# Kernel tuning notes

Measured on AMD Instinct MI355X. Metric: run time of the kernel, lower is better.

Reference implementation:

```python
import jax, jax.numpy as jnp
import numpy as np

NUM_SUBSET = 3
BN_EPS = 1e-5


def setup_inputs() -> dict:
    key = jax.random.key(0)
    ks = jax.random.split(key, 6)
    N, C, T, V = 32, 192, 256, 25
    x = jax.random.normal(ks[0], (N, C, T, V), dtype=jnp.float32)
    w_in = jax.random.normal(ks[1], (3 * C, C), dtype=jnp.float32) * (1.0 / np.sqrt(C))
    b_in = jax.random.normal(ks[2], (3 * C,), dtype=jnp.float32) * 0.02
    w_ff = jax.random.normal(ks[3], (C, C), dtype=jnp.float32) * (1.0 / np.sqrt(C))
    b_ff = jax.random.normal(ks[4], (C,), dtype=jnp.float32) * 0.02
    bn_gamma = jnp.ones((C,), dtype=jnp.float32)
    bn_beta = jnp.zeros((C,), dtype=jnp.float32)
    bn_mean = jnp.zeros((C,), dtype=jnp.float32)
    bn_var = jnp.ones((C,), dtype=jnp.float32)
    return dict(x=x, w_in=w_in, b_in=b_in, w_ff=w_ff, b_ff=b_ff,
                bn_gamma=bn_gamma, bn_beta=bn_beta, bn_mean=bn_mean, bn_var=bn_var)


def reference(x, w_in, b_in, w_ff, b_ff, bn_gamma, bn_beta, bn_mean, bn_var):
    N, C, T, V = x.shape
    S = NUM_SUBSET
    mid = C // S
    # 1x1 conv QKV projection: (N,C,T,V) x (3C,C) -> (N,3C,T,V)
    qkv = jnp.einsum('nctv,dc->ndtv', x, w_in) + b_in[None, :, None, None]
    qkv = qkv.reshape(N, 3 * S, mid, T, V)
    q, k, v = jnp.split(qkv, 3, axis=1)  # each (N,S,mid,T,V)
    # tanh-normalized attention over time: (N,S,T,T)
    att = jnp.tanh(jnp.einsum('nsctv,nscqv->nstq', q, k) / (mid * V))
    y = jnp.einsum('nstq,nscqv->nsctv', att, v).reshape(N, C, T, V)
    # ff_nett: 1x1 conv + BatchNorm (inference form)
    y = jnp.einsum('nctv,dc->ndtv', y, w_ff) + b_ff[None, :, None, None]
    inv = bn_gamma / jnp.sqrt(bn_var + BN_EPS)
    y = (y - bn_mean[None, :, None, None]) * inv[None, :, None, None] + bn_beta[None, :, None, None]
    # residual + LeakyReLU(0.1)
    z = x + y
    return jnp.where(z >= 0, z, 0.1 * z)
```

## Files before the change

kernel.cpp:

```cpp
#include <hip/hip_runtime.h>

#define TV 6400
#define NCH 192
#define D3 576

typedef unsigned short u16;
typedef unsigned int   u32;

typedef __attribute__((ext_vector_type(8))) short bf16x8;
typedef __attribute__((ext_vector_type(4))) float f32x4;

__device__ __forceinline__ float bf2f(u32 h) { return __uint_as_float(h << 16); }
__device__ __forceinline__ u16 f2bf(float f) {
    u32 u = __float_as_uint(f);
    return (u16)((u + 0x7FFFu + ((u >> 16) & 1u)) >> 16);
}

__global__ __launch_bounds__(256) void k_wcast(const float* __restrict__ w_in,
                                               const float* __restrict__ w_ff,
                                               u32* __restrict__ wb) {
    int i = blockIdx.x * 256 + threadIdx.x;
    float2 f;
    if (i < 55296) f = *(const float2*)(w_in + 2 * i);
    else           f = *(const float2*)(w_ff + 2 * (i - 55296));
    wb[i] = (u32)f2bf(f.x) | ((u32)f2bf(f.y) << 16);
}

__global__ __launch_bounds__(256) void k_qkv(const float* __restrict__ x,
                                             const u16* __restrict__ w_inb,
                                             const float* __restrict__ b_in,
                                             u16* __restrict__ qkv,
                                             u16* __restrict__ qt,
                                             u16* __restrict__ kt) {
    const int p0 = blockIdx.x * 64, n = blockIdx.y;
    const int tid = threadIdx.x;
    const int wid = tid >> 6, lane = tid & 63;
    const int wd = wid & 1, wp = wid >> 1;
    const int ml = lane & 15, kq = lane >> 4;

    __shared__ __align__(16) char Bs[64 * 384];
    __shared__ __align__(16) char As[64 * 384];
    float* L = (float*)As;

    for (int cc = 0; cc < 3; ++cc) {
        const float* xn = x + ((size_t)n * NCH + cc * 64) * TV + p0;
#pragma unroll
        for (int r = 0; r < 4; ++r) {
            int idx = tid + 256 * r;
            int c = idx >> 4, p4 = idx & 15;
            float4 v = *(const float4*)(xn + (size_t)c * TV + p4 * 4);
            *(float4*)&L[c * 65 + p4 * 4] = v;
        }
        __syncthreads();
        {
            int p = tid >> 2, cq = tid & 3;
            u32 buf[8];
#pragma unroll
            for (int j = 0; j < 8; ++j) {
                float f0 = L[(cq * 16 + 2 * j) * 65 + p];
                float f1 = L[(cq * 16 + 2 * j + 1) * 65 + p];
                buf[j] = (u32)f2bf(f0) | ((u32)f2bf(f1) << 16);
            }
#pragma unroll
            for (int h = 0; h < 2; ++h) {
                int g = cc * 8 + cq * 2 + h;
                uint4 u;
                u.x = buf[h * 4]; u.y = buf[h * 4 + 1];
                u.z = buf[h * 4 + 2]; u.w = buf[h * 4 + 3];
                *(uint4*)(Bs + p * 384 + (((g & ~7) | ((g ^ p) & 7)) << 4)) = u;
            }
        }
        __syncthreads();
    }

    for (int dt = 0; dt < 9; ++dt) {
#pragma unroll
        for (int r = 0; r < 6; ++r) {
            int idx = tid + 256 * r;
            int row = idx / 24, g = idx - row * 24;
            uint4 v = *(const uint4*)(w_inb + (size_t)(dt * 64 + row) * 192 + g * 8);
            *(uint4*)(As + row * 384 + (((g & ~7) | ((g ^ row) & 7)) << 4)) = v;
        }
        __syncthreads();

        f32x4 acc[2][2];
#pragma unroll
        for (int i = 0; i < 2; i++)
#pragma unroll
            for (int j = 0; j < 2; j++)
#pragma unroll
                for (int r = 0; r < 4; r++) acc[i][j][r] = 0.f;

#pragma unroll
        for (int kk = 0; kk < 3; ++kk)
#pragma unroll
            for (int ks = 0; ks < 2; ++ks) {
                int g = kk * 8 + ks * 4 + kq;
                bf16x8 aw[2], bx[2];
#pragma unroll
                for (int mt = 0; mt < 2; ++mt) {
                    int row = wd * 32 + mt * 16 + ml;
                    aw[mt] = *(const bf16x8*)(As + row * 384 + (((g & ~7) | ((g ^ row) & 7)) << 4));
                }
#pragma unroll
                for (int nt = 0; nt < 2; ++nt) {
                    int row = wp * 32 + nt * 16 + ml;
                    bx[nt] = *(const bf16x8*)(Bs + row * 384 + (((g & ~7) | ((g ^ row) & 7)) << 4));
                }
#pragma unroll
                for (int mt = 0; mt < 2; ++mt)
#pragma unroll
                    for (int nt = 0; nt < 2; ++nt)
                        acc[mt][nt] = __builtin_amdgcn_mfma_f32_16x16x32_bf16(aw[mt], bx[nt], acc[mt][nt], 0, 0, 0);
            }

        if (dt < 6) {
            const int s = (dt < 3) ? dt : dt - 3;
            u16* dstb = (dt < 3 ? qt : kt) + ((size_t)(n * 3 + s) * 6400 + p0) * 64;
#pragma unroll
            for (int mt = 0; mt < 2; ++mt) {
                int c = wd * 32 + mt * 16 + kq * 4;
                float4 bias = *(const float4*)(b_in + dt * 64 + c);
#pragma unroll
                for (int nt = 0; nt < 2; ++nt) {
                    int p = wp * 32 + nt * 16 + ml;
                    u32 w0 = (u32)f2bf(acc[mt][nt][0] + bias.x) | ((u32)f2bf(acc[mt][nt][1] + bias.y) << 16);
                    u32 w1 = (u32)f2bf(acc[mt][nt][2] + bias.z) | ((u32)f2bf(acc[mt][nt][3] + bias.w) << 16);
                    uint2 u; u.x = w0; u.y = w1;
                    *(uint2*)(dstb + (size_t)p * 64 + c) = u;
                }
            }
        } else {
#pragma unroll
            for (int mt = 0; mt < 2; ++mt) {
                int d = dt * 64 + wd * 32 + mt * 16 + kq * 4;
                float4 bias = *(const float4*)(b_in + d);
                u16* vdst = qkv + ((size_t)n * D3 + d) * TV;
#pragma unroll
                for (int nt = 0; nt < 2; ++nt) {
                    int p = p0 + wp * 32 + nt * 16 + ml;
                    vdst[(size_t)0 * TV + p] = f2bf(acc[mt][nt][0] + bias.x);
                    vdst[(size_t)1 * TV + p] = f2bf(acc[mt][nt][1] + bias.y);
                    vdst[(size_t)2 * TV + p] = f2bf(acc[mt][nt][2] + bias.z);
                    vdst[(size_t)3 * TV + p] = f2bf(acc[mt][nt][3] + bias.w);
                }
            }
        }
        __syncthreads();
    }
}

__global__ __launch_bounds__(256) void k_scores(const u16* __restrict__ qt,
                                                const u16* __restrict__ kt,
                                                u16* __restrict__ att) {
    const int b = blockIdx.z, t0 = blockIdx.y * 128, q0 = blockIdx.x * 64;
    const int tid = threadIdx.x;
    const int wid = tid >> 6, lane = tid & 63;
    const int wm = wid & 1, wn = wid >> 1;
    const int ml = lane & 15, kq = lane >> 4;

    __shared__ __align__(16) char As[128 * 128];
    __shared__ __align__(16) char Bs[64 * 128];

    f32x4 acc[4][2];
#pragma unroll
    for (int i = 0; i < 4; i++)
#pragma unroll
        for (int j = 0; j < 2; j++)
#pragma unroll
            for (int r = 0; r < 4; r++) acc[i][j][r] = 0.f;

    const u16* qb = qt + (size_t)b * 256 * 1600;
    const u16* kb = kt + (size_t)b * 256 * 1600;

    for (int kc = 0; kc < 1600; kc += 64) {
#pragma unroll
        for (int r = 0; r < 4; r++) {
            int idx = tid + 256 * r;
            int row = idx >> 3, g = idx & 7;
            uint4 v = *(const uint4*)(qb + (size_t)(t0 + row) * 1600 + kc + g * 8);
            *(uint4*)(As + row * 128 + (((g ^ row) & 7) << 4)) = v;
        }
#pragma unroll
        for (int r = 0; r < 2; r++) {
            int idx = tid + 256 * r;
            int row = idx >> 3, g = idx & 7;
            uint4 v = *(const uint4*)(kb + (size_t)(q0 + row) * 1600 + kc + g * 8);
            *(uint4*)(Bs + row * 128 + (((g ^ row) & 7) << 4)) = v;
        }
        __syncthreads();
#pragma unroll
        for (int ks = 0; ks < 2; ks++) {
            int gb = ks * 4 + kq;
            bf16x8 a[4], bb[2];
#pragma unroll
            for (int mt = 0; mt < 4; mt++) {
                int row = wm * 64 + mt * 16 + ml;
                a[mt] = *(const bf16x8*)(As + row * 128 + (((gb ^ row) & 7) << 4));
            }
#pragma unroll
            for (int nt = 0; nt < 2; nt++) {
                int row = wn * 32 + nt * 16 + ml;
                bb[nt] = *(const bf16x8*)(Bs + row * 128 + (((gb ^ row) & 7) << 4));
            }
#pragma unroll
            for (int mt = 0; mt < 4; mt++)
#pragma unroll
                for (int nt = 0; nt < 2; nt++)
                    acc[mt][nt] = __builtin_amdgcn_mfma_f32_16x16x32_bf16(a[mt], bb[nt], acc[mt][nt], 0, 0, 0);
        }
        __syncthreads();
    }

    const float sc = 1.0f / 1600.0f;
    u16* ab = att + (size_t)b * 65536;
#pragma unroll
    for (int mt = 0; mt < 4; mt++)
#pragma unroll
        for (int nt = 0; nt < 2; nt++) {
            int q = q0 + wn * 32 + nt * 16 + ml;
#pragma unroll
            for (int r = 0; r < 4; r++) {
                int t = t0 + wm * 64 + mt * 16 + kq * 4 + r;
                ab[(size_t)t * 256 + q] = f2bf(tanhf(acc[mt][nt][r] * sc));
            }
        }
}

__global__ __launch_bounds__(256) void k_trv(const u16* __restrict__ qkv,
                                             u16* __restrict__ vt) {
    const int q0 = blockIdx.x * 32;
    const int c0 = blockIdx.y * 32;
    const int b  = blockIdx.z;
    const int n = b / 3, s = b % 3;
    const int tid = threadIdx.x;

    __shared__ u16 L[32 * 800];

    const u16* src = qkv + ((size_t)n * D3 + 384 + s * 64 + c0) * TV + q0 * 25;
#pragma unroll
    for (int r = 0; r < 13; ++r) {
        int idx = tid + 256 * r;
        if (idx < 3200) {
            int c = idx / 100, w = idx - 100 * c;
            uint4 v = *(const uint4*)(src + (size_t)c * TV + w * 8);
            *(uint4*)&L[c * 800 + w * 8] = v;
        }
    }
    __syncthreads();

    u16* dst = vt + ((size_t)b * 1600 + c0) * 256 + q0;
#pragma unroll
    for (int r = 0; r < 4; ++r) {
        int idx = tid + 256 * r;
        if (idx < 800) {
            int c = idx / 25, v = idx - 25 * c;
            const u16* lp = &L[c * 800 + v];
            u32 buf[16];
#pragma unroll
            for (int j = 0; j < 16; ++j) {
                u32 lo = lp[(2 * j) * 25];
                u32 hi = lp[(2 * j + 1) * 25];
                buf[j] = lo | (hi << 16);
            }
            u16* dp = dst + (size_t)(v * 64 + c) * 256;
#pragma unroll
            for (int q4 = 0; q4 < 4; ++q4) {
                uint4 u; u.x = buf[q4 * 4]; u.y = buf[q4 * 4 + 1];
                u.z = buf[q4 * 4 + 2]; u.w = buf[q4 * 4 + 3];
                *(uint4*)(dp + q4 * 8) = u;
            }
        }
    }
}

__global__ __launch_bounds__(256) void k_av(const u16* __restrict__ att,
                                            const u16* __restrict__ vt,
                                            u16* __restrict__ y_t) {
    const int b = blockIdx.z, t0 = blockIdx.y * 128, v = blockIdx.x;
    const int n = b / 3, s = b % 3;
    const int tid = threadIdx.x;
    const int wid = tid >> 6, lane = tid & 63;
    const int wm = wid & 1, wn = wid >> 1;
    const int ml = lane & 15, kq = lane >> 4;

    __shared__ __align__(16) char As[128 * 128];
    __shared__ __align__(16) char Bs[64 * 128];

    f32x4 acc[4][2];
#pragma unroll
    for (int i = 0; i < 4; i++)
#pragma unroll
        for (int j = 0; j < 2; j++)
#pragma unroll
            for (int r = 0; r < 4; r++) acc[i][j][r] = 0.f;

    const u16* ab = att + (size_t)b * 65536;
    const u16* vb = vt + ((size_t)b * 1600 + v * 64) * 256;

    for (int kc = 0; kc < 256; kc += 64) {
#pragma unroll
        for (int r = 0; r < 4; r++) {
            int idx = tid + 256 * r;
            int row = idx >> 3, g = idx & 7;
            uint4 u = *(const uint4*)(ab + (size_t)(t0 + row) * 256 + kc + g * 8);
            *(uint4*)(As + row * 128 + (((g ^ row) & 7) << 4)) = u;
        }
#pragma unroll
        for (int r = 0; r < 2; r++) {
            int idx = tid + 256 * r;
            int row = idx >> 3, g = idx & 7;
            uint4 u = *(const uint4*)(vb + (size_t)row * 256 + kc + g * 8);
            *(uint4*)(Bs + row * 128 + (((g ^ row) & 7) << 4)) = u;
        }
        __syncthreads();
#pragma unroll
        for (int ks = 0; ks < 2; ks++) {
            int gb = ks * 4 + kq;
            bf16x8 a[4], bb[2];
#pragma unroll
            for (int mt = 0; mt < 4; mt++) {
                int row = wm * 64 + mt * 16 + ml;
                a[mt] = *(const bf16x8*)(As + row * 128 + (((gb ^ row) & 7) << 4));
            }
#pragma unroll
            for (int nt = 0; nt < 2; nt++) {
                int row = wn * 32 + nt * 16 + ml;
                bb[nt] = *(const bf16x8*)(Bs + row * 128 + (((gb ^ row) & 7) << 4));
            }
#pragma unroll
            for (int mt = 0; mt < 4; mt++)
#pragma unroll
                for (int nt = 0; nt < 2; nt++)
                    acc[mt][nt] = __builtin_amdgcn_mfma_f32_16x16x32_bf16(a[mt], bb[nt], acc[mt][nt], 0, 0, 0);
        }
        __syncthreads();
    }

#pragma unroll
    for (int mt = 0; mt < 4; mt++)
#pragma unroll
        for (int nt = 0; nt < 2; nt++) {
            int cg = s * 64 + wn * 32 + nt * 16 + ml;
#pragma unroll
            for (int r = 0; r < 4; r++) {
                int t = t0 + wm * 64 + mt * 16 + kq * 4 + r;
                y_t[((size_t)n * TV + t * 25 + v) * 192 + cg] = f2bf(acc[mt][nt][r]);
            }
        }
}

__global__ __launch_bounds__(256) void k_ff(const u16* __restrict__ y_t,
                                            const float* __restrict__ x,
                                            const u16* __restrict__ w_ffb,
                                            const float* __restrict__ b_ff,
                                            const float* __restrict__ gamma,
                                            const float* __restrict__ beta,
                                            const float* __restrict__ mean,
                                            const float* __restrict__ var,
                                            float* __restrict__ out) {
    const int n = blockIdx.z, d0 = blockIdx.y * 64, p0 = blockIdx.x * 128;
    const int tid = threadIdx.x;
    const int wid = tid >> 6, lane = tid & 63;
    const int wn = wid;
    const int ml = lane & 15, kq = lane >> 4;

    __shared__ __align__(16) char Aw[64 * 128];
    __shared__ __align__(16) char By[128 * 128];

    f32x4 acc[4][2];
#pragma unroll
    for (int i = 0; i < 4; i++)
#pragma unroll
        for (int j = 0; j < 2; j++)
#pragma unroll
            for (int r = 0; r < 4; r++) acc[i][j][r] = 0.f;

    for (int kc = 0; kc < 192; kc += 64) {
#pragma unroll
        for (int r = 0; r < 2; r++) {
            int idx = tid + 256 * r;
            int row = idx >> 3, g = idx & 7;
            uint4 v = *(const uint4*)(w_ffb + (size_t)(d0 + row) * 192 + kc + g * 8);
            *(uint4*)(Aw + row * 128 + (((g ^ row) & 7) << 4)) = v;
        }
#pragma unroll
        for (int r = 0; r < 4; r++) {
            int idx = tid + 256 * r;
            int row = idx >> 3, g = idx & 7;
            uint4 v = *(const uint4*)(y_t + ((size_t)n * TV + p0 + row) * 192 + kc + g * 8);
            *(uint4*)(By + row * 128 + (((g ^ row) & 7) << 4)) = v;
        }
        __syncthreads();
#pragma unroll
        for (int ks = 0; ks < 2; ks++) {
            int gb = ks * 4 + kq;
            bf16x8 a[4], bb[2];
#pragma unroll
            for (int mt = 0; mt < 4; mt++) {
                int row = mt * 16 + ml;
                a[mt] = *(const bf16x8*)(Aw + row * 128 + (((gb ^ row) & 7) << 4));
            }
#pragma unroll
            for (int nt = 0; nt < 2; nt++) {
                int row = wn * 32 + nt * 16 + ml;
                bb[nt] = *(const bf16x8*)(By + row * 128 + (((gb ^ row) & 7) << 4));
            }
#pragma unroll
            for (int mt = 0; mt < 4; mt++)
#pragma unroll
                for (int nt = 0; nt < 2; nt++)
                    acc[mt][nt] = __builtin_amdgcn_mfma_f32_16x16x32_bf16(a[mt], bb[nt], acc[mt][nt], 0, 0, 0);
        }
        __syncthreads();
    }

#pragma unroll
    for (int mt = 0; mt < 4; mt++)
#pragma unroll
        for (int r = 0; r < 4; r++) {
            int d = d0 + mt * 16 + kq * 4 + r;
            float inv = gamma[d] * rsqrtf(var[d] + 1e-5f);
            float bias = b_ff[d], mu = mean[d], bt = beta[d];
#pragma unroll
            for (int nt = 0; nt < 2; nt++) {
                int p = p0 + wn * 32 + nt * 16 + ml;
                size_t xi = ((size_t)n * NCH + d) * TV + p;
                float v = acc[mt][nt][r] + bias;
                v = (v - mu) * inv + bt;
                float z = x[xi] + v;
                out[xi] = (z >= 0.f) ? z : 0.1f * z;
            }
        }
}

extern "C" void kernel_launch(void* const* d_in, const int* in_sizes, int n_in,
                              void* d_out, int out_size, void* d_ws, size_t ws_size,
                              hipStream_t stream) {
    const float* x     = (const float*)d_in[0];
    const float* w_in  = (const float*)d_in[1];
    const float* b_in  = (const float*)d_in[2];
    const float* w_ff  = (const float*)d_in[3];
    const float* b_ff  = (const float*)d_in[4];
    const float* gamma = (const float*)d_in[5];
    const float* beta  = (const float*)d_in[6];
    const float* mean  = (const float*)d_in[7];
    const float* var   = (const float*)d_in[8];

    u16* qkv = (u16*)d_ws;
    u16* att = (u16*)((char*)d_ws + 235929600ull);
    u16* y_t = (u16*)((char*)d_ws + 248512512ull);
    u32* wb  = (u32*)((char*)d_ws + 327155712ull);
    u16* w_inb = (u16*)wb;
    u16* w_ffb = w_inb + 110592;
    u16* qt = (u16*)d_out;
    u16* kt = qt + 39321600ull;
    u16* vt = qt;
    float* out = (float*)d_out;

    k_wcast <<<dim3(288),        dim3(256), 0, stream>>>(w_in, w_ff, wb);
    k_qkv   <<<dim3(100, 32),    dim3(256), 0, stream>>>(x, w_inb, b_in, qkv, qt, kt);
    k_scores<<<dim3(4, 2, 96),   dim3(256), 0, stream>>>(qt, kt, att);
    k_trv   <<<dim3(8, 2, 96),   dim3(256), 0, stream>>>(qkv, vt);
    k_av    <<<dim3(25, 2, 96),  dim3(256), 0, stream>>>(att, vt, y_t);
    k_ff    <<<dim3(50, 3, 32),  dim3(256), 0, stream>>>(y_t, x, w_ffb, b_ff, gamma, beta, mean, var, out);
}
```

Measured before the change: 598.5 us.

## Enlarge score tiles to 128x128 and keep y tile resident across output channels

The score GEMM now computes 128x128 output tiles per block instead of 128x64, halving the number of blocks and reusing each loaded Q tile across twice as many K rows. The feed-forward kernel loads the full 128-position by 192-channel y tile into shared memory once and loops over the three 64-channel output slices inside the block, instead of launching separate blocks per slice that each reload y. This cuts redundant global loads of y and Q, but raises shared memory and register use per block, which lowers occupancy. The score grid shrinks to 384 blocks, which may underfill the GPU.

```diff
diff --git a/kernel.cpp b/kernel.cpp
--- a/kernel.cpp
+++ b/kernel.cpp
@@ -153,20 +153,20 @@
 __global__ __launch_bounds__(256) void k_scores(const u16* __restrict__ qt,
                                                 const u16* __restrict__ kt,
                                                 u16* __restrict__ att) {
-    const int b = blockIdx.z, t0 = blockIdx.y * 128, q0 = blockIdx.x * 64;
+    const int b = blockIdx.z, t0 = blockIdx.y * 128, q0 = blockIdx.x * 128;
     const int tid = threadIdx.x;
     const int wid = tid >> 6, lane = tid & 63;
     const int wm = wid & 1, wn = wid >> 1;
     const int ml = lane & 15, kq = lane >> 4;
 
     __shared__ __align__(16) char As[128 * 128];
-    __shared__ __align__(16) char Bs[64 * 128];
-
-    f32x4 acc[4][2];
+    __shared__ __align__(16) char Bs[128 * 128];
+
+    f32x4 acc[4][4];
 #pragma unroll
     for (int i = 0; i < 4; i++)
 #pragma unroll
-        for (int j = 0; j < 2; j++)
+        for (int j = 0; j < 4; j++)
 #pragma unroll
             for (int r = 0; r < 4; r++) acc[i][j][r] = 0.f;
 
@@ -182,7 +182,7 @@
             *(uint4*)(As + row * 128 + (((g ^ row) & 7) << 4)) = v;
         }
 #pragma unroll
-        for (int r = 0; r < 2; r++) {
+        for (int r = 0; r < 4; r++) {
             int idx = tid + 256 * r;
             int row = idx >> 3, g = idx & 7;
             uint4 v = *(const uint4*)(kb + (size_t)(q0 + row) * 1600 + kc + g * 8);
@@ -192,21 +192,21 @@
 #pragma unroll
         for (int ks = 0; ks < 2; ks++) {
             int gb = ks * 4 + kq;
-            bf16x8 a[4], bb[2];
+            bf16x8 a[4], bb[4];
 #pragma unroll
             for (int mt = 0; mt < 4; mt++) {
                 int row = wm * 64 + mt * 16 + ml;
                 a[mt] = *(const bf16x8*)(As + row * 128 + (((gb ^ row) & 7) << 4));
             }
 #pragma unroll
-            for (int nt = 0; nt < 2; nt++) {
-                int row = wn * 32 + nt * 16 + ml;
+            for (int nt = 0; nt < 4; nt++) {
+                int row = wn * 64 + nt * 16 + ml;
                 bb[nt] = *(const bf16x8*)(Bs + row * 128 + (((gb ^ row) & 7) << 4));
             }
 #pragma unroll
             for (int mt = 0; mt < 4; mt++)
 #pragma unroll
-                for (int nt = 0; nt < 2; nt++)
+                for (int nt = 0; nt < 4; nt++)
                     acc[mt][nt] = __builtin_amdgcn_mfma_f32_16x16x32_bf16(a[mt], bb[nt], acc[mt][nt], 0, 0, 0);
         }
         __syncthreads();
@@ -217,8 +217,8 @@
 #pragma unroll
     for (int mt = 0; mt < 4; mt++)
 #pragma unroll
-        for (int nt = 0; nt < 2; nt++) {
-            int q = q0 + wn * 32 + nt * 16 + ml;
+        for (int nt = 0; nt < 4; nt++) {
+            int q = q0 + wn * 64 + nt * 16 + ml;
 #pragma unroll
             for (int r = 0; r < 4; r++) {
                 int t = t0 + wm * 64 + mt * 16 + kq * 4 + r;
@@ -359,79 +359,83 @@
                                             const float* __restrict__ mean,
                                             const float* __restrict__ var,
                                             float* __restrict__ out) {
-    const int n = blockIdx.z, d0 = blockIdx.y * 64, p0 = blockIdx.x * 128;
+    const int n = blockIdx.y, p0 = blockIdx.x * 128;
     const int tid = threadIdx.x;
     const int wid = tid >> 6, lane = tid & 63;
     const int wn = wid;
     const int ml = lane & 15, kq = lane >> 4;
 
-    __shared__ __align__(16) char Aw[64 * 128];
-    __shared__ __align__(16) char By[128 * 128];
-
-    f32x4 acc[4][2];
-#pragma unroll
-    for (int i = 0; i < 4; i++)
-#pragma unroll
-        for (int j = 0; j < 2; j++)
-#pragma unroll
-            for (int r = 0; r < 4; r++) acc[i][j][r] = 0.f;
-
-    for (int kc = 0; kc < 192; kc += 64) {
-#pragma unroll
-        for (int r = 0; r < 2; r++) {
-            int idx = tid + 256 * r;
-            int row = idx >> 3, g = idx & 7;
-            uint4 v = *(const uint4*)(w_ffb + (size_t)(d0 + row) * 192 + kc + g * 8);
-            *(uint4*)(Aw + row * 128 + (((g ^ row) & 7) << 4)) = v;
-        }
-#pragma unroll
-        for (int r = 0; r < 4; r++) {
-            int idx = tid + 256 * r;
-            int row = idx >> 3, g = idx & 7;
-            uint4 v = *(const uint4*)(y_t + ((size_t)n * TV + p0 + row) * 192 + kc + g * 8);
-            *(uint4*)(By + row * 128 + (((g ^ row) & 7) << 4)) = v;
-        }
-        __syncthreads();
-#pragma unroll
-        for (int ks = 0; ks < 2; ks++) {
-            int gb = ks * 4 + kq;
-            bf16x8 a[4], bb[2];
-#pragma unroll
-            for (int mt = 0; mt < 4; mt++) {
-                int row = mt * 16 + ml;
-                a[mt] = *(const bf16x8*)(Aw + row * 128 + (((gb ^ row) & 7) << 4));
-            }
-#pragma unroll
-            for (int nt = 0; nt < 2; nt++) {
-                int row = wn * 32 + nt * 16 + ml;
-                bb[nt] = *(const bf16x8*)(By + row * 128 + (((gb ^ row) & 7) << 4));
-            }
-#pragma unroll
-            for (int mt = 0; mt < 4; mt++)
-#pragma unroll
-                for (int nt = 0; nt < 2; nt++)
-                    acc[mt][nt] = __builtin_amdgcn_mfma_f32_16x16x32_bf16(a[mt], bb[nt], acc[mt][nt], 0, 0, 0);
-        }
-        __syncthreads();
-    }
-
-#pragma unroll
-    for (int mt = 0; mt < 4; mt++)
-#pragma unroll
-        for (int r = 0; r < 4; r++) {
-            int d = d0 + mt * 16 + kq * 4 + r;
-            float inv = gamma[d] * rsqrtf(var[d] + 1e-5f);
-            float bias = b_ff[d], mu = mean[d], bt = beta[d];
-#pragma unroll
-            for (int nt = 0; nt < 2; nt++) {
-                int p = p0 + wn * 32 + nt * 16 + ml;
-                size_t xi = ((size_t)n * NCH + d) * TV + p;
-                float v = acc[mt][nt][r] + bias;
-                v = (v - mu) * inv + bt;
-                float z = x[xi] + v;
-                out[xi] = (z >= 0.f) ? z : 0.1f * z;
-            }
-        }
+    __shared__ __align__(16) char Aw[64 * 384];
+    __shared__ __align__(16) char By[128 * 384];
+
+#pragma unroll
+    for (int r = 0; r < 12; ++r) {
+        int idx = tid + 256 * r;
+        int row = idx / 24, g = idx - row * 24;
+        uint4 v = *(const uint4*)(y_t + ((size_t)n * TV + p0 + row) * 192 + g * 8);
+        *(uint4*)(By + row * 384 + (((g & ~7) | ((g ^ row) & 7)) << 4)) = v;
+    }
+
+    for (int dt = 0; dt < 3; ++dt) {
+#pragma unroll
+        for (int r = 0; r < 6; ++r) {
+            int idx = tid + 256 * r;
+            int row = idx / 24, g = idx - row * 24;
+            uint4 v = *(const uint4*)(w_ffb + (size_t)(dt * 64 + row) * 192 + g * 8);
+            *(uint4*)(Aw + row * 384 + (((g & ~7) | ((g ^ row) & 7)) << 4)) = v;
+        }
+        __syncthreads();
+
+        f32x4 acc[4][2];
+#pragma unroll
+        for (int i = 0; i < 4; i++)
+#pragma unroll
+            for (int j = 0; j < 2; j++)
+#pragma unroll
+                for (int r = 0; r < 4; r++) acc[i][j][r] = 0.f;
+
+#pragma unroll
+        for (int kk = 0; kk < 3; ++kk)
+#pragma unroll
+            for (int ks = 0; ks < 2; ++ks) {
+                int g = kk * 8 + ks * 4 + kq;
+                bf16x8 a[4], bb[2];
+#pragma unroll
+                for (int mt = 0; mt < 4; mt++) {
+                    int row = mt * 16 + ml;
+                    a[mt] = *(const bf16x8*)(Aw + row * 384 + (((g & ~7) | ((g ^ row) & 7)) << 4));
+                }
+#pragma unroll
+                for (int nt = 0; nt < 2; nt++) {
+                    int row = wn * 32 + nt * 16 + ml;
+                    bb[nt] = *(const bf16x8*)(By + row * 384 + (((g & ~7) | ((g ^ row) & 7)) << 4));
+                }
+#pragma unroll
+                for (int mt = 0; mt < 4; mt++)
+#pragma unroll
+                    for (int nt = 0; nt < 2; nt++)
+                        acc[mt][nt] = __builtin_amdgcn_mfma_f32_16x16x32_bf16(a[mt], bb[nt], acc[mt][nt], 0, 0, 0);
+            }
+
+#pragma unroll
+        for (int mt = 0; mt < 4; mt++)
+#pragma unroll
+            for (int r = 0; r < 4; r++) {
+                int d = dt * 64 + mt * 16 + kq * 4 + r;
+                float inv = gamma[d] * rsqrtf(var[d] + 1e-5f);
+                float bias = b_ff[d], mu = mean[d], bt = beta[d];
+#pragma unroll
+                for (int nt = 0; nt < 2; nt++) {
+                    int p = p0 + wn * 32 + nt * 16 + ml;
+                    size_t xi = ((size_t)n * NCH + d) * TV + p;
+                    float v = acc[mt][nt][r] + bias;
+                    v = (v - mu) * inv + bt;
+                    float z = x[xi] + v;
+                    out[xi] = (z >= 0.f) ? z : 0.1f * z;
+                }
+            }
+        __syncthreads();
+    }
 }
 
 extern "C" void kernel_launch(void* const* d_in, const int* in_sizes, int n_in,
@@ -460,8 +464,8 @@
 
     k_wcast <<<dim3(288),        dim3(256), 0, stream>>>(w_in, w_ff, wb);
     k_qkv   <<<dim3(100, 32),    dim3(256), 0, stream>>>(x, w_inb, b_in, qkv, qt, kt);
-    k_scores<<<dim3(4, 2, 96),   dim3(256), 0, stream>>>(qt, kt, att);
+    k_scores<<<dim3(2, 2, 96),   dim3(256), 0, stream>>>(qt, kt, att);
     k_trv   <<<dim3(8, 2, 96),   dim3(256), 0, stream>>>(qkv, vt);
     k_av    <<<dim3(25, 2, 96),  dim3(256), 0, stream>>>(att, vt, y_t);
-    k_ff    <<<dim3(50, 3, 32),  dim3(256), 0, stream>>>(y_t, x, w_ffb, b_ff, gamma, beta, mean, var, out);
-}
+    k_ff    <<<dim3(50, 32),     dim3(256), 0, stream>>>(y_t, x, w_ffb, b_ff, gamma, beta, mean, var, out);
+}
```

Result: faster. 584.8 us, median of 2 (-2.3%).
